# Performance work log

Hardware: AMD Instinct MI355X
Metric: run time of the kernel (lower is better)

Reference implementation:

```python
import jax, jax.numpy as jnp
import numpy as np

H = 1024       # hidden_size
R = 4          # downsacale_ratio -> bottleneck H//R = 256
DI = 2048      # mamba d_inner = expand * H
NS = 16        # d_state
KC = 4         # d_conv
DTR = 64       # dt_rank = ceil(H/16)
B, L = 4, 1024


def setup_inputs() -> dict:
    key = jax.random.key(0)
    ks = iter(jax.random.split(key, 32))
    w = lambda shape, s=0.02: jax.random.normal(next(ks), shape, jnp.float32) * s
    Hr = H // R
    inp = {
        'x': jax.random.normal(next(ks), (B, L, H), jnp.float32),
        't': jax.random.normal(next(ks), (B, H), jnp.float32),
        # adaLN modulation: SiLU -> Linear(H, 3H)
        'ada_w': w((H, 3 * H)), 'ada_b': jnp.zeros((3 * H,), jnp.float32),
        # hg_dense: Linear(H,H/R) SiLU Linear(H/R,H)
        'hgd_w1': w((H, Hr)), 'hgd_b1': jnp.zeros((Hr,), jnp.float32),
        'hgd_w2': w((Hr, H)), 'hgd_b2': jnp.zeros((H,), jnp.float32),
        # Mamba params
        'in_proj_w': w((H, 2 * DI)),
        'conv_w': w((DI, KC), 0.1), 'conv_b': jnp.zeros((DI,), jnp.float32),
        'x_proj_w': w((DI, DTR + 2 * NS)),
        'dt_proj_w': w((DTR, DI), 0.1),
        'dt_proj_b': jnp.log(jnp.expm1(jnp.full((DI,), 0.01, jnp.float32))),  # softplus^-1(0.01)
        'A_log': jnp.log(jnp.broadcast_to(jnp.arange(1, NS + 1, dtype=jnp.float32), (DI, NS))),
        'Dp': jnp.ones((DI,), jnp.float32),
        'out_proj_w': w((DI, H)),
        # hg_fuse
        'fm_w': w((H, Hr)), 'fm_b': jnp.zeros((Hr,), jnp.float32),
        'fr_w': w((H, Hr)), 'fr_b': jnp.zeros((Hr,), jnp.float32),
        'ff_w': w((Hr, H)), 'ff_b': jnp.zeros((H,), jnp.float32),
    }
    return inp


def _ln(x, eps=1e-6):
    mu = jnp.mean(x, -1, keepdims=True)
    var = jnp.mean(jnp.square(x - mu), -1, keepdims=True)
    return (x - mu) / jnp.sqrt(var + eps)


def _mamba(xd, in_proj_w, conv_w, conv_b, x_proj_w, dt_proj_w, dt_proj_b, A_log, Dp, out_proj_w):
    # xd: [B, L, H]
    xz = xd @ in_proj_w                      # [B, L, 2*DI]
    xm, z = jnp.split(xz, 2, axis=-1)
    # causal depthwise conv over time
    xc = jnp.swapaxes(xm, 1, 2)              # [B, DI, L]
    xc = jax.lax.conv_general_dilated(
        xc, conv_w[:, None, :], window_strides=(1,), padding=[(KC - 1, 0)],
        feature_group_count=DI, dimension_numbers=('NCH', 'OIH', 'NCH'))
    xc = jax.nn.silu(jnp.swapaxes(xc, 1, 2) + conv_b)   # [B, L, DI]
    dbl = xc @ x_proj_w                      # [B, L, DTR + 2*NS]
    dt = jax.nn.softplus(dbl[..., :DTR] @ dt_proj_w + dt_proj_b)   # [B, L, DI]
    Bm = dbl[..., DTR:DTR + NS]              # [B, L, NS]
    Cm = dbl[..., DTR + NS:]                 # [B, L, NS]
    A = -jnp.exp(A_log)                      # [DI, NS]

    def step(h, inp):
        dt_t, x_t, B_t, C_t = inp            # [B,DI],[B,DI],[B,NS],[B,NS]
        dA = jnp.exp(dt_t[:, :, None] * A)                       # [B, DI, NS]
        h = dA * h + (dt_t * x_t)[:, :, None] * B_t[:, None, :]
        y = jnp.einsum('bdn,bn->bd', h, C_t)
        return h, y

    h0 = jnp.zeros((xd.shape[0], DI, NS), xd.dtype)
    seq = (jnp.moveaxis(dt, 1, 0), jnp.moveaxis(xc, 1, 0),
           jnp.moveaxis(Bm, 1, 0), jnp.moveaxis(Cm, 1, 0))
    _, ys = jax.lax.scan(step, h0, seq)
    y = jnp.moveaxis(ys, 0, 1) + xc * Dp     # [B, L, DI]
    y = y * jax.nn.silu(z)
    return y @ out_proj_w                    # [B, L, H]


def reference(x, t, ada_w, ada_b, hgd_w1, hgd_b1, hgd_w2, hgd_b2,
              in_proj_w, conv_w, conv_b, x_proj_w, dt_proj_w, dt_proj_b,
              A_log, Dp, out_proj_w, fm_w, fm_b, fr_w, fr_b, ff_w, ff_b):
    ada = jax.nn.silu(t) @ ada_w + ada_b               # [B, 3H]
    shift, scale, alpha = jnp.split(ada, 3, axis=-1)
    x1 = _ln(x) * (1 + scale[:, None, :]) + shift[:, None, :]
    xd = jax.nn.silu(x1 @ hgd_w1 + hgd_b1) @ hgd_w2 + hgd_b2
    x1_2 = _mamba(xd, in_proj_w, conv_w, conv_b, x_proj_w, dt_proj_w,
                  dt_proj_b, A_log, Dp, out_proj_w)
    a = jax.nn.silu(x1_2 @ fm_w + fm_b)
    b = jax.nn.silu(x1 @ fr_w + fr_b)
    fuse = (a * b) @ ff_w + ff_b
    return x + alpha[:, None, :] * fuse
```

## Files before the change

### kernel.cpp

```cpp
#include <hip/hip_runtime.h>
#include <math.h>
#include <stdint.h>

#define H_   1024
#define HR_  256
#define DI_  2048
#define NS_  16
#define KC_  4
#define DTR_ 64
#define B_   4
#define L_   1024
#define ROWS (B_*L_)
#define H3_  3072
#define NCH_ 32
#define CL_  32
#define CLT_ 8

typedef short bf16x8 __attribute__((ext_vector_type(8)));
typedef float f32x4  __attribute__((ext_vector_type(4)));

#if __has_builtin(__builtin_amdgcn_exp2f)
#define EXP2(x) __builtin_amdgcn_exp2f(x)
#else
#define EXP2(x) __expf((x) * 0.6931471805599453f)
#endif
#define LOG2E 1.4426950408889634f

__device__ __forceinline__ float silu_f(float v) { return v / (1.f + __expf(-v)); }

__device__ __forceinline__ uint32_t pack_bf16_2(float a, float b) {
    uint32_t ua = __float_as_uint(a);
    uint32_t ub = __float_as_uint(b);
    uint32_t ra = (ua + 0x7FFFu + ((ua >> 16) & 1u)) >> 16;
    uint32_t rb = (ub + 0x7FFFu + ((ub >> 16) & 1u)) >> 16;
    return ra | (rb << 16);
}
__device__ __forceinline__ unsigned short cvt_bf16(float a) {
    uint32_t ua = __float_as_uint(a);
    return (unsigned short)((ua + 0x7FFFu + ((ua >> 16) & 1u)) >> 16);
}
__device__ __forceinline__ float bf16_to_f(unsigned short u) {
    return __uint_as_float(((uint32_t)u) << 16);
}

__device__ __forceinline__ void gload16(const short* g, short* l) {
    __builtin_amdgcn_global_load_lds(
        (const __attribute__((address_space(1))) void*)g,
        (__attribute__((address_space(3))) void*)l, 16, 0, 0);
}

#define TW_HGDFR 0ull
#define TW_HGD2  524288ull
#define TW_INPJ  786432ull
#define TW_XPJ   4980736ull
#define TW_DTPJ  5242880ull
#define TW_OPJ   5373952ull
#define TW_FM    7471104ull
#define TW_FF    7733248ull
#define TWT      7995392ull

__global__ __launch_bounds__(256) void wtrans_kernel(
    const float* __restrict__ s0, const float* __restrict__ s1,
    const float* __restrict__ s2, const float* __restrict__ s3,
    const float* __restrict__ s4, const float* __restrict__ s5,
    const float* __restrict__ s6, const float* __restrict__ s7,
    const float* __restrict__ s8, short* __restrict__ wt)
{
    int bid = blockIdx.x;
    const float* src; short* dst; int K, N, rel;
    if      (bid < 256)  { src = s0; dst = wt + TW_HGDFR;          K = 1024; N = 256;  rel = bid; }
    else if (bid < 512)  { src = s1; dst = wt + TW_HGDFR + 262144; K = 1024; N = 256;  rel = bid - 256; }
    else if (bid < 768)  { src = s2; dst = wt + TW_HGD2;           K = 256;  N = 1024; rel = bid - 512; }
    else if (bid < 4864) { src = s3; dst = wt + TW_INPJ;           K = 1024; N = 4096; rel = bid - 768; }
    else if (bid < 5120) { src = s4; dst = wt + TW_XPJ;            K = 2048; N = 96;   rel = bid - 4864; }
    else if (bid < 5248) { src = s5; dst = wt + TW_DTPJ;           K = 64;   N = 2048; rel = bid - 5120; }
    else if (bid < 7296) { src = s6; dst = wt + TW_OPJ;            K = 2048; N = 1024; rel = bid - 5248; }
    else if (bid < 7552) { src = s7; dst = wt + TW_FM;             K = 1024; N = 256;  rel = bid - 7296; }
    else                 { src = s8; dst = wt + TW_FF;             K = 256;  N = 1024; rel = bid - 7552; }
    int tkc = K >> 5;
    int tk = rel % tkc, tn = rel / tkc;

    __shared__ float ld[32][33];
    int tx = threadIdx.x & 7, ty = threadIdx.x >> 3;
    int kk = tk * 32 + ty, nn = tn * 32 + tx * 4;
    float4 v = make_float4(0.f, 0.f, 0.f, 0.f);
    if (nn < N) v = *(const float4*)&src[(size_t)kk * N + nn];
    ld[ty][tx * 4 + 0] = v.x; ld[ty][tx * 4 + 1] = v.y;
    ld[ty][tx * 4 + 2] = v.z; ld[ty][tx * 4 + 3] = v.w;
    __syncthreads();
    int nn2 = tn * 32 + ty, kk2 = tk * 32 + tx * 4;
    float a0 = ld[tx * 4 + 0][ty], a1 = ld[tx * 4 + 1][ty];
    float a2 = ld[tx * 4 + 2][ty], a3 = ld[tx * 4 + 3][ty];
    uint2 p = { pack_bf16_2(a0, a1), pack_bf16_2(a2, a3) };
    *(uint2*)&dst[(size_t)nn2 * K + kk2] = p;
}

__global__ __launch_bounds__(256) void cwt_kernel(
    const float* __restrict__ conv_w, float* __restrict__ cwt)
{
    int d = blockIdx.x * 256 + threadIdx.x;
    float4 v = *(const float4*)&conv_w[d * KC_];
    cwt[0 * DI_ + d] = v.x;
    cwt[1 * DI_ + d] = v.y;
    cwt[2 * DI_ + d] = v.z;
    cwt[3 * DI_ + d] = v.w;
}

__global__ __launch_bounds__(256) void ada_part_kernel(
    const float* __restrict__ t, const float* __restrict__ ada_w,
    float* __restrict__ part)
{
    int col = blockIdx.x * 1024 + threadIdx.x * 4;
    int b = blockIdx.y, z = blockIdx.z;
    __shared__ float st[32];
    if (threadIdx.x < 32) {
        float v = t[b * H_ + z * 32 + threadIdx.x];
        st[threadIdx.x] = silu_f(v);
    }
    __syncthreads();
    float4 acc = make_float4(0.f, 0.f, 0.f, 0.f);
    const float* w = ada_w + (size_t)(z * 32) * H3_ + col;
    #pragma unroll
    for (int k = 0; k < 32; ++k) {
        float4 wv = *(const float4*)(w + (size_t)k * H3_);
        float s = st[k];
        acc.x = fmaf(s, wv.x, acc.x);
        acc.y = fmaf(s, wv.y, acc.y);
        acc.z = fmaf(s, wv.z, acc.z);
        acc.w = fmaf(s, wv.w, acc.w);
    }
    *(float4*)&part[((size_t)z * B_ + b) * H3_ + col] = acc;
}

__global__ __launch_bounds__(256) void ada_red_kernel(
    const float* __restrict__ part, const float* __restrict__ ada_b,
    float* __restrict__ ada)
{
    int i = (blockIdx.x * 256 + threadIdx.x) * 4;
    int b = i / H3_, col = i - b * H3_;
    float4 s = make_float4(0.f, 0.f, 0.f, 0.f);
    #pragma unroll
    for (int z = 0; z < 32; ++z) {
        float4 p = *(const float4*)&part[((size_t)z * B_ + b) * H3_ + col];
        s.x += p.x; s.y += p.y; s.z += p.z; s.w += p.w;
    }
    float4 bv = *(const float4*)&ada_b[col];
    s.x += bv.x; s.y += bv.y; s.z += bv.z; s.w += bv.w;
    *(float4*)&ada[(size_t)b * H3_ + col] = s;
}

__global__ __launch_bounds__(256) void ln_mod_kernel(
    const float* __restrict__ x, const float* __restrict__ ada,
    short* __restrict__ x1b)
{
    int row = blockIdx.x;
    int b   = row >> 10;
    const float* xr = x + (size_t)row * H_;
    float4 v = ((const float4*)xr)[threadIdx.x];
    float s  = v.x + v.y + v.z + v.w;
    float s2 = v.x*v.x + v.y*v.y + v.z*v.z + v.w*v.w;

    __shared__ float red[8];
    int wave = threadIdx.x >> 6, lane = threadIdx.x & 63;
    #pragma unroll
    for (int off = 32; off; off >>= 1) {
        s  += __shfl_down(s,  off);
        s2 += __shfl_down(s2, off);
    }
    if (lane == 0) { red[wave] = s; red[4 + wave] = s2; }
    __syncthreads();
    float ts  = red[0] + red[1] + red[2] + red[3];
    float ts2 = red[4] + red[5] + red[6] + red[7];
    float mu  = ts  * (1.f / H_);
    float var = ts2 * (1.f / H_) - mu * mu;
    float inv = rsqrtf(var + 1e-6f);

    const float* sh = ada + b * H3_;
    int i = threadIdx.x * 4;
    float4 sh4 = *(const float4*)&sh[i];
    float4 sc4 = *(const float4*)&sh[H_ + i];
    float ox = (v.x - mu) * inv * (1.f + sc4.x) + sh4.x;
    float oy = (v.y - mu) * inv * (1.f + sc4.y) + sh4.y;
    float oz = (v.z - mu) * inv * (1.f + sc4.z) + sh4.z;
    float ow = (v.w - mu) * inv * (1.f + sc4.w) + sh4.w;
    uint2 p = { pack_bf16_2(ox, oy), pack_bf16_2(oz, ow) };
    *(uint2*)(x1b + (size_t)row * H_ + i) = p;
}

template<int ACT, bool SPLITK>
__global__ __launch_bounds__(256) void gemm128(
    const short* __restrict__ A, int lda,
    const short* __restrict__ Wt, int ldw,
    const float* __restrict__ bias,
    float* __restrict__ C, short* __restrict__ Cb, short* __restrict__ Cb2,
    int ldc, int M, int N, int K,
    const float* __restrict__ E0, const float* __restrict__ E1)
{
    __shared__ short As[3][4096];
    __shared__ short Bs[3][4096];
    int tid  = threadIdx.x;
    int lane = tid & 63, wv = tid >> 6, wm = wv >> 1, wn = wv & 1;
    int n0 = blockIdx.x * 128;
    int m0 = blockIdx.y * 128;

    if (SPLITK) {
        int z = blockIdx.z;
        A  += (size_t)z * K;
        Wt += (size_t)z * K;
        C  += (size_t)z * M * N;
    }

    int r = lane & 15, g = lane >> 4;
    int sA = wv * 2;
    const short* ga0 = A  + (size_t)(m0 + sA * 16 + r) * lda + g * 8;
    const short* ga1 = ga0 + (size_t)16 * lda;
    const short* gb0 = Wt + (size_t)(n0 + sA * 16 + r) * ldw + g * 8;
    const short* gb1 = gb0 + (size_t)16 * ldw;

    f32x4 acc[4][4];
    #pragma unroll
    for (int i = 0; i < 4; ++i)
        #pragma unroll
        for (int j = 0; j < 4; ++j) {
            acc[i][j][0] = 0.f; acc[i][j][1] = 0.f;
            acc[i][j][2] = 0.f; acc[i][j][3] = 0.f;
        }

    #define STAGE(buf, koff)                                    \
        do {                                                    \
            gload16(ga0 + (koff), &As[buf][sA * 512]);          \
            gload16(ga1 + (koff), &As[buf][sA * 512 + 512]);    \
            gload16(gb0 + (koff), &Bs[buf][sA * 512]);          \
            gload16(gb1 + (koff), &Bs[buf][sA * 512 + 512]);    \
        } while (0)

    #define COMPUTE(buf)                                                          \
        do {                                                                      \
            bf16x8 af[4], bfr[4];                                                 \
            _Pragma("unroll")                                                     \
            for (int i = 0; i < 4; ++i)                                           \
                af[i] = *(const bf16x8*)&As[buf][(wm * 4 + i) * 512 + lane * 8];  \
            _Pragma("unroll")                                                     \
            for (int j = 0; j < 4; ++j)                                           \
                bfr[j] = *(const bf16x8*)&Bs[buf][(wn * 4 + j) * 512 + lane * 8]; \
            _Pragma("unroll")                                                     \
            for (int i = 0; i < 4; ++i)                                           \
                _Pragma("unroll")                                                 \
                for (int j = 0; j < 4; ++j)                                       \
                    acc[i][j] = __builtin_amdgcn_mfma_f32_16x16x32_bf16(          \
                        af[i], bfr[j], acc[i][j], 0, 0, 0);                       \
        } while (0)

    int T = K >> 5;
    STAGE(0, 0);
    if (T > 1) STAGE(1, 32);
    for (int t = 0; t < T; ++t) {
        if (t + 1 < T) asm volatile("s_waitcnt vmcnt(4)" ::: "memory");
        else           asm volatile("s_waitcnt vmcnt(0)" ::: "memory");
        __builtin_amdgcn_s_barrier();
        if (t + 2 < T) STAGE((t + 2) % 3, (t + 2) * 32);
        COMPUTE(t % 3);
    }
    #undef STAGE
    #undef COMPUTE

    #pragma unroll
    for (int i = 0; i < 4; ++i) {
        int mb = m0 + wm * 64 + i * 16 + ((lane >> 4) << 2);
        #pragma unroll
        for (int j = 0; j < 4; ++j) {
            int n = n0 + wn * 64 + j * 16 + (lane & 15);
            if (n < N) {
                float bv;
                if (ACT == 6) bv = (n < 256) ? bias[n] : E0[n - 256];
                else          bv = bias ? bias[n] : 0.f;
                #pragma unroll
                for (int rr = 0; rr < 4; ++rr) {
                    int m = mb + rr;
                    float v = acc[i][j][rr] + bv;
                    size_t ci = (size_t)m * ldc + n;
                    if (ACT == 6) {
                        float sv = silu_f(v);
                        if (n < 256) Cb[(size_t)m * 256 + n]        = (short)cvt_bf16(sv);
                        else         Cb2[(size_t)m * 256 + (n-256)] = (short)cvt_bf16(sv);
                    } else {
                        if (ACT == 2) v = (v > 20.f) ? v : log1pf(__expf(v));
                        else if (ACT == 4) {
                            int bb = m >> 10;
                            v = E0[ci] + E1[bb * H3_ + 2 * H_ + n] * v;
                        }
                        if (C)  C[ci]  = v;
                        if (Cb) Cb[ci] = (short)cvt_bf16(v);
                    }
                }
            }
        }
    }
}

template<int ACT>
__global__ __launch_bounds__(512) void gemm256(
    const short* __restrict__ A, int lda,
    const short* __restrict__ Wt, int ldw,
    short* __restrict__ Cb, int M, int N, int K)
{
    extern __shared__ short lds[];
    short* Asb = lds;
    short* Bsb = lds + 24576;
    int tid  = threadIdx.x;
    int lane = tid & 63, wv = tid >> 6;
    int wm = wv >> 2, wn = wv & 3;
    int n0 = blockIdx.x * 256;
    int m0 = blockIdx.y * 256;

    int r = lane & 15, g = lane >> 4;
    int sA = wv * 2;
    const short* ga0 = A  + (size_t)(m0 + sA * 16 + r) * lda + g * 8;
    const short* ga1 = ga0 + (size_t)16 * lda;
    const short* gb0 = Wt + (size_t)(n0 + sA * 16 + r) * ldw + g * 8;
    const short* gb1 = gb0 + (size_t)16 * ldw;

    f32x4 acc[8][4];
    #pragma unroll
    for (int i = 0; i < 8; ++i)
        #pragma unroll
        for (int j = 0; j < 4; ++j) {
            acc[i][j][0] = 0.f; acc[i][j][1] = 0.f;
            acc[i][j][2] = 0.f; acc[i][j][3] = 0.f;
        }

    #define STAGE2(buf, koff)                                       \
        do {                                                        \
            gload16(ga0 + (koff), &Asb[(buf) * 8192 + sA * 512]);   \
            gload16(ga1 + (koff), &Asb[(buf) * 8192 + sA * 512 + 512]); \
            gload16(gb0 + (koff), &Bsb[(buf) * 8192 + sA * 512]);   \
            gload16(gb1 + (koff), &Bsb[(buf) * 8192 + sA * 512 + 512]); \
        } while (0)

    int T = K >> 5;
    STAGE2(0, 0);
    if (T > 1) STAGE2(1, 32);
    for (int t = 0; t < T; ++t) {
        if (t + 1 < T) asm volatile("s_waitcnt vmcnt(4)" ::: "memory");
        else           asm volatile("s_waitcnt vmcnt(0)" ::: "memory");
        __builtin_amdgcn_s_barrier();
        if (t + 2 < T) STAGE2((t + 2) % 3, (t + 2) * 32);
        {
            int buf = t % 3;
            bf16x8 af[8], bfr[4];
            #pragma unroll
            for (int i = 0; i < 8; ++i)
                af[i] = *(const bf16x8*)&Asb[buf * 8192 + (wm * 8 + i) * 512 + lane * 8];
            #pragma unroll
            for (int j = 0; j < 4; ++j)
                bfr[j] = *(const bf16x8*)&Bsb[buf * 8192 + (wn * 4 + j) * 512 + lane * 8];
            __builtin_amdgcn_s_setprio(1);
            #pragma unroll
            for (int i = 0; i < 8; ++i)
                #pragma unroll
                for (int j = 0; j < 4; ++j)
                    acc[i][j] = __builtin_amdgcn_mfma_f32_16x16x32_bf16(
                        af[i], bfr[j], acc[i][j], 0, 0, 0);
            __builtin_amdgcn_s_setprio(0);
        }
    }
    #undef STAGE2

    #pragma unroll
    for (int i = 0; i < 8; ++i) {
        int mb = m0 + wm * 128 + i * 16 + ((lane >> 4) << 2);
        #pragma unroll
        for (int j = 0; j < 4; ++j) {
            int n = n0 + wn * 64 + j * 16 + (lane & 15);
            #pragma unroll
            for (int rr = 0; rr < 4; ++rr) {
                int m = mb + rr;
                float v = acc[i][j][rr];
                if (ACT == 5) {
                    size_t idx = (n < DI_) ? ((size_t)m * DI_ + n)
                                           : ((size_t)ROWS * DI_ + (size_t)m * DI_ + (n - DI_));
                    Cb[idx] = (short)cvt_bf16(v);
                }
            }
        }
    }
}

__global__ __launch_bounds__(256) void redk_xproj(
    const float* __restrict__ part, float* __restrict__ dbl,
    short* __restrict__ dblb)
{
    size_t i = ((size_t)blockIdx.x * 256 + threadIdx.x) * 4;
    const size_t seg = (size_t)ROWS * 96;
    float4 s = *(const float4*)(part + i);
    #pragma unroll
    for (int z = 1; z < 8; ++z) {
        float4 p = *(const float4*)(part + z * seg + i);
        s.x += p.x; s.y += p.y; s.z += p.z; s.w += p.w;
    }
    *(float4*)(dbl + i) = s;
    uint2 p = { pack_bf16_2(s.x, s.y), pack_bf16_2(s.z, s.w) };
    *(uint2*)(dblb + i) = p;
}

__global__ __launch_bounds__(256) void redk_op(
    const float* __restrict__ part, short* __restrict__ x12b)
{
    size_t i = ((size_t)blockIdx.x * 256 + threadIdx.x) * 4;
    const size_t seg = (size_t)ROWS * H_;
    float4 a = *(const float4*)(part + i);
    float4 b = *(const float4*)(part + seg + i);
    uint2 p = { pack_bf16_2(a.x + b.x, a.y + b.y), pack_bf16_2(a.z + b.z, a.w + b.w) };
    *(uint2*)(x12b + i) = p;
}

__global__ __launch_bounds__(256) void redk_fm(
    const float* __restrict__ part, const float* __restrict__ fm_b,
    const short* __restrict__ frlin, short* __restrict__ abb)
{
    size_t i = ((size_t)blockIdx.x * 256 + threadIdx.x) * 4;
    const size_t seg = (size_t)ROWS * HR_;
    float4 s = *(const float4*)(part + i);
    #pragma unroll
    for (int z = 1; z < 4; ++z) {
        float4 p = *(const float4*)(part + z * seg + i);
        s.x += p.x; s.y += p.y; s.z += p.z; s.w += p.w;
    }
    int col = (int)(i & (HR_ - 1));
    float4 b = *(const float4*)(fm_b + col);
    const short* fr = frlin + i;
    float o0 = silu_f(s.x + b.x) * bf16_to_f((unsigned short)fr[0]);
    float o1 = silu_f(s.y + b.y) * bf16_to_f((unsigned short)fr[1]);
    float o2 = silu_f(s.z + b.z) * bf16_to_f((unsigned short)fr[2]);
    float o3 = silu_f(s.w + b.w) * bf16_to_f((unsigned short)fr[3]);
    uint2 p = { pack_bf16_2(o0, o1), pack_bf16_2(o2, o3) };
    *(uint2*)(abb + i) = p;
}

__global__ __launch_bounds__(256) void conv_kernel(
    const short* __restrict__ xmb, const float* __restrict__ cwt,
    const float* __restrict__ conv_b, short* __restrict__ xcb)
{
    int d0 = threadIdx.x * 8;
    int b  = blockIdx.y;
    int l0 = blockIdx.x * CLT_;

    float w[KC_][8];
    #pragma unroll
    for (int j = 0; j < KC_; ++j) {
        float4 a = *(const float4*)&cwt[j * DI_ + d0];
        float4 c = *(const float4*)&cwt[j * DI_ + d0 + 4];
        w[j][0] = a.x; w[j][1] = a.y; w[j][2] = a.z; w[j][3] = a.w;
        w[j][4] = c.x; w[j][5] = c.y; w[j][6] = c.z; w[j][7] = c.w;
    }
    float bia[8];
    {
        float4 b0 = *(const float4*)&conv_b[d0];
        float4 b1 = *(const float4*)&conv_b[d0 + 4];
        bia[0] = b0.x; bia[1] = b0.y; bia[2] = b0.z; bia[3] = b0.w;
        bia[4] = b1.x; bia[5] = b1.y; bia[6] = b1.z; bia[7] = b1.w;
    }

    const short* base = xmb + (size_t)b * L_ * DI_ + d0;
    short*       outb = xcb + (size_t)b * L_ * DI_ + d0;

    bf16x8 win[KC_];
    #pragma unroll
    for (int j = 0; j < KC_ - 1; ++j) {
        int ll = l0 - (KC_ - 1) + j;
        if (ll >= 0) win[j] = *(const bf16x8*)(base + (size_t)ll * DI_);
        else         win[j] = (bf16x8)0;
    }
    for (int l = l0; l < l0 + CLT_; ++l) {
        win[KC_ - 1] = *(const bf16x8*)(base + (size_t)l * DI_);
        bf16x8 o;
        #pragma unroll
        for (int e = 0; e < 8; ++e) {
            float acc = bia[e];
            #pragma unroll
            for (int j = 0; j < KC_; ++j)
                acc = fmaf(bf16_to_f((unsigned short)win[j][e]), w[j][e], acc);
            o[e] = (short)cvt_bf16(silu_f(acc));
        }
        *(bf16x8*)(outb + (size_t)l * DI_) = o;
        win[0] = win[1]; win[1] = win[2]; win[2] = win[3];
    }
}

__global__ __launch_bounds__(256) void scan_part1(
    const short* __restrict__ dtb, const short* __restrict__ xcb,
    const float* __restrict__ dbl, const float* __restrict__ A_log,
    float* __restrict__ hend, float* __restrict__ dtsum)
{
    int bx = blockIdx.x;
    int dg = bx & 15;
    int bc = bx >> 4;
    int c  = bc & (NCH_ - 1);
    int b  = bc >> 5;
    int tid  = threadIdx.x;
    int lane = tid & 63, wv = tid >> 6;
    int dl   = tid >> 1;
    int d    = dg * 128 + dl;
    int half = tid & 1;
    int n0   = half * 8;

    __shared__ float sB[CL_][NS_];
    __shared__ short dtS[2][16][128];
    __shared__ short xcS[2][16][128];

    size_t srcoff = (size_t)(b * L_ + c * CL_ + wv * 4 + (lane >> 4)) * DI_
                    + dg * 128 + (lane & 15) * 8;
    const short* gdt = dtb + srcoff;
    const short* gxc = xcb + srcoff;

    #define SSTG1(buf, q)                                             \
        do {                                                          \
            gload16(gdt + (size_t)(q) * 16 * DI_, &dtS[buf][wv*4][0]); \
            gload16(gxc + (size_t)(q) * 16 * DI_, &xcS[buf][wv*4][0]); \
        } while (0)

    SSTG1(0, 0);
    for (int idx = tid; idx < CL_ * NS_; idx += 256) {
        int l = idx >> 4, n = idx & 15;
        sB[l][n] = dbl[(size_t)(b * L_ + c * CL_ + l) * 96 + DTR_ + n];
    }
    float Aa2[8];
    #pragma unroll
    for (int n = 0; n < 8; ++n)
        Aa2[n] = -__expf(A_log[d * NS_ + n0 + n]) * LOG2E;

    float h[8];
    #pragma unroll
    for (int n = 0; n < 8; ++n) h[n] = 0.f;
    float sdt = 0.f;

    __syncthreads();
    int buf = 0;
    for (int q = 0; q < 2; ++q) {
        if (q < 1) SSTG1(buf ^ 1, q + 1);
        #pragma unroll
        for (int li = 0; li < 16; ++li) {
            int l = q * 16 + li;
            float dtv = bf16_to_f((unsigned short)dtS[buf][li][dl]);
            float xv  = bf16_to_f((unsigned short)xcS[buf][li][dl]);
            float du  = dtv * xv;
            sdt += dtv;
            #pragma unroll
            for (int n = 0; n < 8; ++n)
                h[n] = fmaf(EXP2(dtv * Aa2[n]), h[n], du * sB[l][n0 + n]);
        }
        __syncthreads();
        buf ^= 1;
    }
    #undef SSTG1

    #pragma unroll
    for (int n = 0; n < 8; ++n)
        hend[((size_t)((b * NCH_ + c) * NS_ + n0 + n)) * DI_ + d] = h[n];
    if (half == 0)
        dtsum[(size_t)(b * NCH_ + c) * DI_ + d] = sdt;
}

__global__ __launch_bounds__(256) void scan_mid(
    const float* __restrict__ hend, const float* __restrict__ dtsum,
    const float* __restrict__ A_log, float* __restrict__ hin)
{
    int idx = blockIdx.x * 256 + threadIdx.x;
    int d  = idx & (DI_ - 1);
    int bn = idx >> 11;
    int n  = bn & (NS_ - 1);
    int b  = bn >> 4;
    float Aa2 = -__expf(A_log[d * NS_ + n]) * LOG2E;
    float h = 0.f;
    #pragma unroll
    for (int c = 0; c < NCH_; ++c) {
        size_t o = ((size_t)((b * NCH_ + c) * NS_ + n)) * DI_ + d;
        hin[o] = h;
        float s = dtsum[(size_t)(b * NCH_ + c) * DI_ + d];
        h = fmaf(EXP2(Aa2 * s), h, hend[o]);
    }
}

__global__ __launch_bounds__(256) void scan_part2(
    const short* __restrict__ dtb, const short* __restrict__ xcb,
    const short* __restrict__ zb, const float* __restrict__ dbl,
    const float* __restrict__ A_log, const float* __restrict__ Dp,
    const float* __restrict__ hin, short* __restrict__ y2b)
{
    int bx = blockIdx.x;
    int dg = bx & 15;
    int bc = bx >> 4;
    int c  = bc & (NCH_ - 1);
    int b  = bc >> 5;
    int tid  = threadIdx.x;
    int lane = tid & 63, wv = tid >> 6;
    int dl   = tid >> 1;
    int d    = dg * 128 + dl;
    int half = tid & 1;
    int n0   = half * 8;

    __shared__ float sBC[CL_][2 * NS_];
    __shared__ short dtS[2][16][128];
    __shared__ short xcS[2][16][128];
    __shared__ short zS[2][16][128];

    size_t srcoff = (size_t)(b * L_ + c * CL_ + wv * 4 + (lane >> 4)) * DI_
                    + dg * 128 + (lane & 15) * 8;
    const short* gdt = dtb + srcoff;
    const short* gxc = xcb + srcoff;
    const short* gz  = zb  + srcoff;

    #define SSTG2(buf, q)                                             \
        do {                                                          \
            gload16(gdt + (size_t)(q) * 16 * DI_, &dtS[buf][wv*4][0]); \
            gload16(gxc + (size_t)(q) * 16 * DI_, &xcS[buf][wv*4][0]); \
            gload16(gz  + (size_t)(q) * 16 * DI_, &zS[buf][wv*4][0]);  \
        } while (0)

    SSTG2(0, 0);
    for (int idx = tid; idx < CL_ * 2 * NS_; idx += 256) {
        int l = idx >> 5, n = idx & 31;
        sBC[l][n] = dbl[(size_t)(b * L_ + c * CL_ + l) * 96 + DTR_ + n];
    }
    float Aa2[8];
    #pragma unroll
    for (int n = 0; n < 8; ++n)
        Aa2[n] = -__expf(A_log[d * NS_ + n0 + n]) * LOG2E;

    float h[8];
    #pragma unroll
    for (int n = 0; n < 8; ++n)
        h[n] = hin[((size_t)((b * NCH_ + c) * NS_ + n0 + n)) * DI_ + d];
    float Dpv = Dp[d];
    size_t obase = (size_t)(b * L_ + c * CL_) * DI_ + d;

    __syncthreads();
    int buf = 0;
    for (int q = 0; q < 2; ++q) {
        if (q < 1) SSTG2(buf ^ 1, q + 1);
        #pragma unroll
        for (int li = 0; li < 16; ++li) {
            int l = q * 16 + li;
            float dtv = bf16_to_f((unsigned short)dtS[buf][li][dl]);
            float xv  = bf16_to_f((unsigned short)xcS[buf][li][dl]);
            float zv  = bf16_to_f((unsigned short)zS[buf][li][dl]);
            float du  = dtv * xv;
            float y = 0.f;
            #pragma unroll
            for (int n = 0; n < 8; ++n) {
                float dA = EXP2(dtv * Aa2[n]);
                h[n] = fmaf(dA, h[n], du * sBC[l][n0 + n]);
                y = fmaf(h[n], sBC[l][NS_ + n0 + n], y);
            }
            y += __shfl_xor(y, 1);
            if (half == 0) {
                y = fmaf(xv, Dpv, y);
                y2b[obase + (size_t)l * DI_] = (short)cvt_bf16(y * silu_f(zv));
            }
        }
        __syncthreads();
        buf ^= 1;
    }
    #undef SSTG2
}

extern "C" void kernel_launch(void* const* d_in, const int* in_sizes, int n_in,
                              void* d_out, int out_size, void* d_ws, size_t ws_size,
                              hipStream_t stream)
{
    const float* x         = (const float*)d_in[0];
    const float* t         = (const float*)d_in[1];
    const float* ada_w     = (const float*)d_in[2];
    const float* ada_b     = (const float*)d_in[3];
    const float* hgd_w1    = (const float*)d_in[4];
    const float* hgd_b1    = (const float*)d_in[5];
    const float* hgd_w2    = (const float*)d_in[6];
    const float* hgd_b2    = (const float*)d_in[7];
    const float* in_proj_w = (const float*)d_in[8];
    const float* conv_w    = (const float*)d_in[9];
    const float* conv_b    = (const float*)d_in[10];
    const float* x_proj_w  = (const float*)d_in[11];
    const float* dt_proj_w = (const float*)d_in[12];
    const float* dt_proj_b = (const float*)d_in[13];
    const float* A_log     = (const float*)d_in[14];
    const float* Dp        = (const float*)d_in[15];
    const float* out_proj_w= (const float*)d_in[16];
    const float* fm_w      = (const float*)d_in[17];
    const float* fm_b      = (const float*)d_in[18];
    const float* fr_w      = (const float*)d_in[19];
    const float* fr_b      = (const float*)d_in[20];
    const float* ff_w      = (const float*)d_in[21];
    const float* ff_b      = (const float*)d_in[22];
    float* out = (float*)d_out;

    char* p = (char*)d_ws;
    auto alloc = [&](size_t bytes) { char* r = p; p += (bytes + 255) & ~255ull; return r; };

    short* wt      = (short*)alloc(TWT * 2);
    float* cwt     = (float*)alloc((size_t)KC_ * DI_ * 4);
    short* x1b     = (short*)alloc((size_t)ROWS * H_ * 2);
    short* h1b     = (short*)alloc((size_t)ROWS * HR_ * 2);
    short* frlin   = (short*)alloc((size_t)ROWS * HR_ * 2);
    short* xdb     = (short*)alloc((size_t)ROWS * H_ * 2);
    short* xmzb    = (short*)alloc((size_t)ROWS * DI_ * 4);
    short* xcb     = (short*)alloc((size_t)ROWS * DI_ * 2);
    short* y2b     = (short*)alloc((size_t)ROWS * DI_ * 2);
    short* dtb     = (short*)alloc((size_t)ROWS * DI_ * 2);
    float* bigpart = (float*)alloc((size_t)2 * ROWS * H_ * 4);
    float* hend    = (float*)alloc((size_t)B_ * NCH_ * NS_ * DI_ * 4);
    float* dbl     = (float*)alloc((size_t)ROWS * 96 * 4);
    short* dblb    = (short*)alloc((size_t)ROWS * 96 * 2);
    short* x12b    = (short*)alloc((size_t)ROWS * H_ * 2);
    short* abb     = (short*)alloc((size_t)ROWS * HR_ * 2);
    float* ada     = (float*)alloc((size_t)B_ * H3_ * 4);

    short* xmb   = xmzb;
    short* zb    = xmzb + (size_t)ROWS * DI_;
    float* dtsum = (float*)abb;
    float* hin   = bigpart;
    float* adapart = bigpart;

    dim3 blk(256), b512(512);

    wtrans_kernel<<<dim3(7808), blk, 0, stream>>>(
        hgd_w1, fr_w, hgd_w2, in_proj_w, x_proj_w, dt_proj_w, out_proj_w,
        fm_w, ff_w, wt);
    cwt_kernel<<<dim3(DI_ / 256), blk, 0, stream>>>(conv_w, cwt);
    ada_part_kernel<<<dim3(3, B_, 32), blk, 0, stream>>>(t, ada_w, adapart);
    ada_red_kernel<<<dim3(B_ * H3_ / 4 / 256), blk, 0, stream>>>(adapart, ada_b, ada);
    ln_mod_kernel<<<dim3(ROWS), blk, 0, stream>>>(x, ada, x1b);
    gemm128<6, false><<<dim3(4, 32), blk, 0, stream>>>(
        x1b, H_, wt + TW_HGDFR, H_, hgd_b1, nullptr, h1b, frlin,
        512, ROWS, 512, H_, fr_b, nullptr);
    gemm128<0, false><<<dim3(8, 32), blk, 0, stream>>>(
        h1b, HR_, wt + TW_HGD2, HR_, hgd_b2, nullptr, xdb, nullptr,
        H_, ROWS, H_, HR_, nullptr, nullptr);
    gemm256<5><<<dim3(16, 16), b512, 98304, stream>>>(
        xdb, H_, wt + TW_INPJ, H_, xmb, ROWS, 2 * DI_, H_);
    conv_kernel<<<dim3(L_ / CLT_, B_), blk, 0, stream>>>(xmb, cwt, conv_b, xcb);
    gemm128<0, true><<<dim3(1, 32, 8), blk, 0, stream>>>(
        xcb, DI_, wt + TW_XPJ, DI_, nullptr, bigpart, nullptr, nullptr,
        96, ROWS, 96, 256, nullptr, nullptr);
    redk_xproj<<<dim3(ROWS * 96 / 4 / 256), blk, 0, stream>>>(bigpart, dbl, dblb);
    gemm128<2, false><<<dim3(16, 32), blk, 0, stream>>>(
        dblb, 96, wt + TW_DTPJ, DTR_, dt_proj_b, nullptr, dtb, nullptr,
        DI_, ROWS, DI_, DTR_, nullptr, nullptr);
    scan_part1<<<dim3(B_ * NCH_ * 16), blk, 0, stream>>>(
        dtb, xcb, dbl, A_log, hend, dtsum);
    scan_mid<<<dim3(B_ * DI_ * NS_ / 256), blk, 0, stream>>>(
        hend, dtsum, A_log, hin);
    scan_part2<<<dim3(B_ * NCH_ * 16), blk, 0, stream>>>(
        dtb, xcb, zb, dbl, A_log, Dp, hin, y2b);
    gemm128<0, true><<<dim3(8, 32, 2), blk, 0, stream>>>(
        y2b, DI_, wt + TW_OPJ, DI_, nullptr, bigpart, nullptr, nullptr,
        H_, ROWS, H_, 1024, nullptr, nullptr);
    redk_op<<<dim3(ROWS * H_ / 4 / 256), blk, 0, stream>>>(bigpart, x12b);
    gemm128<0, true><<<dim3(2, 32, 4), blk, 0, stream>>>(
        x12b, H_, wt + TW_FM, H_, nullptr, bigpart, nullptr, nullptr,
        HR_, ROWS, HR_, 256, nullptr, nullptr);
    redk_fm<<<dim3(ROWS * HR_ / 4 / 256), blk, 0, stream>>>(bigpart, fm_b, frlin, abb);
    gemm128<4, false><<<dim3(8, 32), blk, 0, stream>>>(
        abb, HR_, wt + TW_FF, HR_, ff_b, out, nullptr, nullptr,
        H_, ROWS, H_, HR_, x, ada);
}
```

Baseline: 361.2 us.

## Use K=64 staged 256-tile GEMM for in_proj and split-K 256-tile out_proj

Adds a gemm256k64 variant that stages 64-wide K slices into double-buffered LDS (128 KB) for the in_proj GEMM, halving the number of barrier/stage iterations. The out_proj GEMM switches from a 128-tile split-K=2 kernel to the 256-tile kernel with split-K=4 and fp32 partial outputs, followed by a 4-way reduction kernel. Workspace is consolidated into one scratch buffer sized for four partial outputs. The larger LDS footprint limits occupancy, and the extra split-K partials add memory traffic for the reduction.

```diff
diff --git a/kernel.cpp b/kernel.cpp
--- a/kernel.cpp
+++ b/kernel.cpp
@@ -298,11 +298,12 @@
     }
 }
 
-template<int ACT>
+template<int ACT, bool SPLITK>
 __global__ __launch_bounds__(512) void gemm256(
     const short* __restrict__ A, int lda,
     const short* __restrict__ Wt, int ldw,
-    short* __restrict__ Cb, int M, int N, int K)
+    short* __restrict__ Cb, float* __restrict__ C, int ldc,
+    int M, int N, int K)
 {
     extern __shared__ short lds[];
     short* Asb = lds;
@@ -312,6 +313,13 @@
     int wm = wv >> 2, wn = wv & 3;
     int n0 = blockIdx.x * 256;
     int m0 = blockIdx.y * 256;
+
+    if (SPLITK) {
+        int z = blockIdx.z;
+        A  += (size_t)z * K;
+        Wt += (size_t)z * K;
+        C  += (size_t)z * M * N;
+    }
 
     int r = lane & 15, g = lane >> 4;
     int sA = wv * 2;
@@ -380,6 +388,117 @@
                     size_t idx = (n < DI_) ? ((size_t)m * DI_ + n)
                                            : ((size_t)ROWS * DI_ + (size_t)m * DI_ + (n - DI_));
                     Cb[idx] = (short)cvt_bf16(v);
+                } else if (ACT == 7) {
+                    C[(size_t)m * ldc + n] = v;
+                }
+            }
+        }
+    }
+}
+
+template<int ACT>
+__global__ __launch_bounds__(512) void gemm256k64(
+    const short* __restrict__ A, int lda,
+    const short* __restrict__ Wt, int ldw,
+    short* __restrict__ Cb, int M, int N, int K)
+{
+    extern __shared__ short lds[];
+    short* Asb = lds;
+    short* Bsb = lds + 32768;
+    int tid  = threadIdx.x;
+    int lane = tid & 63, wv = tid >> 6;
+    int wm = wv >> 2, wn = wv & 3;
+    int n0 = blockIdx.x * 256;
+    int m0 = blockIdx.y * 256;
+
+    const short* gaP0; const short* gaP1; const short* gaP2; const short* gaP3;
+    const short* gbP0; const short* gbP1; const short* gbP2; const short* gbP3;
+    int lo0, lo1, lo2, lo3;
+    {
+        int f0 = wv, f1 = 8 + wv, f2 = 16 + wv, f3 = 24 + wv;
+        #define SRC(fi, P, base, ld)                                              \
+            P = base + (size_t)((fi >> 1) * 16 + (lane & 15)) * ld                \
+                     + (fi & 1) * 32 + (lane >> 4) * 8;
+        SRC(f0, gaP0, (A + (size_t)m0 * lda), lda)  lo0 = f0 * 512;
+        SRC(f1, gaP1, (A + (size_t)m0 * lda), lda)  lo1 = f1 * 512;
+        SRC(f2, gaP2, (A + (size_t)m0 * lda), lda)  lo2 = f2 * 512;
+        SRC(f3, gaP3, (A + (size_t)m0 * lda), lda)  lo3 = f3 * 512;
+        SRC(f0, gbP0, (Wt + (size_t)n0 * ldw), ldw)
+        SRC(f1, gbP1, (Wt + (size_t)n0 * ldw), ldw)
+        SRC(f2, gbP2, (Wt + (size_t)n0 * ldw), ldw)
+        SRC(f3, gbP3, (Wt + (size_t)n0 * ldw), ldw)
+        #undef SRC
+    }
+
+    f32x4 acc[8][4];
+    #pragma unroll
+    for (int i = 0; i < 8; ++i)
+        #pragma unroll
+        for (int j = 0; j < 4; ++j) {
+            acc[i][j][0] = 0.f; acc[i][j][1] = 0.f;
+            acc[i][j][2] = 0.f; acc[i][j][3] = 0.f;
+        }
+
+    #define STAGE64(buf, koff)                                  \
+        do {                                                    \
+            gload16(gaP0 + (koff), &Asb[(buf) * 16384 + lo0]);  \
+            gload16(gaP1 + (koff), &Asb[(buf) * 16384 + lo1]);  \
+            gload16(gaP2 + (koff), &Asb[(buf) * 16384 + lo2]);  \
+            gload16(gaP3 + (koff), &Asb[(buf) * 16384 + lo3]);  \
+            gload16(gbP0 + (koff), &Bsb[(buf) * 16384 + lo0]);  \
+            gload16(gbP1 + (koff), &Bsb[(buf) * 16384 + lo1]);  \
+            gload16(gbP2 + (koff), &Bsb[(buf) * 16384 + lo2]);  \
+            gload16(gbP3 + (koff), &Bsb[(buf) * 16384 + lo3]);  \
+        } while (0)
+
+    int T = K >> 6;
+    STAGE64(0, 0);
+    int cur = 0;
+    for (int t = 0; t < T; ++t) {
+        if (t + 1 < T) {
+            STAGE64(cur ^ 1, (t + 1) * 64);
+            asm volatile("s_waitcnt vmcnt(8)" ::: "memory");
+        } else {
+            asm volatile("s_waitcnt vmcnt(0)" ::: "memory");
+        }
+        __builtin_amdgcn_s_barrier();
+        #pragma unroll
+        for (int kh = 0; kh < 2; ++kh) {
+            bf16x8 af[8], bfr[4];
+            #pragma unroll
+            for (int i = 0; i < 8; ++i)
+                af[i] = *(const bf16x8*)&Asb[cur * 16384 + (((wm * 8 + i) << 1) + kh) * 512 + lane * 8];
+            #pragma unroll
+            for (int j = 0; j < 4; ++j)
+                bfr[j] = *(const bf16x8*)&Bsb[cur * 16384 + (((wn * 4 + j) << 1) + kh) * 512 + lane * 8];
+            __builtin_amdgcn_s_setprio(1);
+            #pragma unroll
+            for (int i = 0; i < 8; ++i)
+                #pragma unroll
+                for (int j = 0; j < 4; ++j)
+                    acc[i][j] = __builtin_amdgcn_mfma_f32_16x16x32_bf16(
+                        af[i], bfr[j], acc[i][j], 0, 0, 0);
+            __builtin_amdgcn_s_setprio(0);
+        }
+        __builtin_amdgcn_s_barrier();
+        cur ^= 1;
+    }
+    #undef STAGE64
+
+    #pragma unroll
+    for (int i = 0; i < 8; ++i) {
+        int mb = m0 + wm * 128 + i * 16 + ((lane >> 4) << 2);
+        #pragma unroll
+        for (int j = 0; j < 4; ++j) {
+            int n = n0 + wn * 64 + j * 16 + (lane & 15);
+            #pragma unroll
+            for (int rr = 0; rr < 4; ++rr) {
+                int m = mb + rr;
+                float v = acc[i][j][rr];
+                if (ACT == 5) {
+                    size_t idx = (n < DI_) ? ((size_t)m * DI_ + n)
+                                           : ((size_t)ROWS * DI_ + (size_t)m * DI_ + (n - DI_));
+                    Cb[idx] = (short)cvt_bf16(v);
                 }
             }
         }
@@ -403,14 +522,18 @@
     *(uint2*)(dblb + i) = p;
 }
 
-__global__ __launch_bounds__(256) void redk_op(
+__global__ __launch_bounds__(256) void redk_op4(
     const float* __restrict__ part, short* __restrict__ x12b)
 {
     size_t i = ((size_t)blockIdx.x * 256 + threadIdx.x) * 4;
     const size_t seg = (size_t)ROWS * H_;
-    float4 a = *(const float4*)(part + i);
-    float4 b = *(const float4*)(part + seg + i);
-    uint2 p = { pack_bf16_2(a.x + b.x, a.y + b.y), pack_bf16_2(a.z + b.z, a.w + b.w) };
+    float4 s = *(const float4*)(part + i);
+    #pragma unroll
+    for (int z = 1; z < 4; ++z) {
+        float4 p = *(const float4*)(part + z * seg + i);
+        s.x += p.x; s.y += p.y; s.z += p.z; s.w += p.w;
+    }
+    uint2 p = { pack_bf16_2(s.x, s.y), pack_bf16_2(s.z, s.w) };
     *(uint2*)(x12b + i) = p;
 }
 
@@ -706,8 +829,7 @@
     short* xcb     = (short*)alloc((size_t)ROWS * DI_ * 2);
     short* y2b     = (short*)alloc((size_t)ROWS * DI_ * 2);
     short* dtb     = (short*)alloc((size_t)ROWS * DI_ * 2);
-    float* bigpart = (float*)alloc((size_t)2 * ROWS * H_ * 4);
-    float* hend    = (float*)alloc((size_t)B_ * NCH_ * NS_ * DI_ * 4);
+    float* scratch = (float*)alloc((size_t)4 * ROWS * H_ * 4);
     float* dbl     = (float*)alloc((size_t)ROWS * 96 * 4);
     short* dblb    = (short*)alloc((size_t)ROWS * 96 * 2);
     short* x12b    = (short*)alloc((size_t)ROWS * H_ * 2);
@@ -717,8 +839,12 @@
     short* xmb   = xmzb;
     short* zb    = xmzb + (size_t)ROWS * DI_;
     float* dtsum = (float*)abb;
-    float* hin   = bigpart;
-    float* adapart = bigpart;
+    float* adapart = scratch;
+    float* xppart  = scratch;
+    float* hend    = scratch;
+    float* hin     = scratch + (size_t)B_ * NCH_ * NS_ * DI_;
+    float* oppart  = scratch;
+    float* fmpart  = scratch;
 
     dim3 blk(256), b512(512);
 
@@ -735,13 +861,13 @@
     gemm128<0, false><<<dim3(8, 32), blk, 0, stream>>>(
         h1b, HR_, wt + TW_HGD2, HR_, hgd_b2, nullptr, xdb, nullptr,
         H_, ROWS, H_, HR_, nullptr, nullptr);
-    gemm256<5><<<dim3(16, 16), b512, 98304, stream>>>(
+    gemm256k64<5><<<dim3(16, 16), b512, 131072, stream>>>(
         xdb, H_, wt + TW_INPJ, H_, xmb, ROWS, 2 * DI_, H_);
     conv_kernel<<<dim3(L_ / CLT_, B_), blk, 0, stream>>>(xmb, cwt, conv_b, xcb);
     gemm128<0, true><<<dim3(1, 32, 8), blk, 0, stream>>>(
-        xcb, DI_, wt + TW_XPJ, DI_, nullptr, bigpart, nullptr, nullptr,
+        xcb, DI_, wt + TW_XPJ, DI_, nullptr, xppart, nullptr, nullptr,
         96, ROWS, 96, 256, nullptr, nullptr);
-    redk_xproj<<<dim3(ROWS * 96 / 4 / 256), blk, 0, stream>>>(bigpart, dbl, dblb);
+    redk_xproj<<<dim3(ROWS * 96 / 4 / 256), blk, 0, stream>>>(xppart, dbl, dblb);
     gemm128<2, false><<<dim3(16, 32), blk, 0, stream>>>(
         dblb, 96, wt + TW_DTPJ, DTR_, dt_proj_b, nullptr, dtb, nullptr,
         DI_, ROWS, DI_, DTR_, nullptr, nullptr);
@@ -751,14 +877,13 @@
         hend, dtsum, A_log, hin);
     scan_part2<<<dim3(B_ * NCH_ * 16), blk, 0, stream>>>(
         dtb, xcb, zb, dbl, A_log, Dp, hin, y2b);
-    gemm128<0, true><<<dim3(8, 32, 2), blk, 0, stream>>>(
-        y2b, DI_, wt + TW_OPJ, DI_, nullptr, bigpart, nullptr, nullptr,
-        H_, ROWS, H_, 1024, nullptr, nullptr);
-    redk_op<<<dim3(ROWS * H_ / 4 / 256), blk, 0, stream>>>(bigpart, x12b);
+    gemm256<7, true><<<dim3(4, 16, 4), b512, 98304, stream>>>(
+        y2b, DI_, wt + TW_OPJ, DI_, nullptr, oppart, H_, ROWS, H_, 512);
+    redk_op4<<<dim3(ROWS * H_ / 4 / 256), blk, 0, stream>>>(oppart, x12b);
     gemm128<0, true><<<dim3(2, 32, 4), blk, 0, stream>>>(
-        x12b, H_, wt + TW_FM, H_, nullptr, bigpart, nullptr, nullptr,
+        x12b, H_, wt + TW_FM, H_, nullptr, fmpart, nullptr, nullptr,
         HR_, ROWS, HR_, 256, nullptr, nullptr);
-    redk_fm<<<dim3(ROWS * HR_ / 4 / 256), blk, 0, stream>>>(bigpart, fm_b, frlin, abb);
+    redk_fm<<<dim3(ROWS * HR_ / 4 / 256), blk, 0, stream>>>(fmpart, fm_b, frlin, abb);
     gemm128<4, false><<<dim3(8, 32), blk, 0, stream>>>(
         abb, HR_, wt + TW_FF, HR_, ff_b, out, nullptr, nullptr,
         H_, ROWS, H_, HR_, x, ada);
```

Result: no change. 359.9 us (-0.4%).

## Use 256-tile double-buffered GEMM with 4-way split-K bf16 partials for out_proj

Applied to the files above, without the earlier changes.

The 256x256 GEMM now uses two LDS buffers with __syncthreads instead of a three-stage vmcnt-gated pipeline, cutting LDS from 96KB to 64KB. The same kernel gains a split-K mode that runs out_proj as 4 K-slices of 512, writing bf16 partial sums. A new reducer sums the four bf16 partials into x12b, replacing the fp32 two-way split-K reducer. Workspace buffers are merged into one scratch region. The aim is larger tiles and less reduction traffic for out_proj, at the cost of extra bf16 rounding in the partials and a shallower in_proj pipeline.

```diff
diff --git a/kernel.cpp b/kernel.cpp
--- a/kernel.cpp
+++ b/kernel.cpp
@@ -298,20 +298,28 @@
     }
 }
 
-template<int ACT>
-__global__ __launch_bounds__(512) void gemm256(
+template<int ACT, bool SPLITK>
+__global__ __launch_bounds__(512) void gemm256d(
     const short* __restrict__ A, int lda,
     const short* __restrict__ Wt, int ldw,
-    short* __restrict__ Cb, int M, int N, int K)
+    short* __restrict__ Cb, int ldc,
+    int M, int N, int K)
 {
     extern __shared__ short lds[];
     short* Asb = lds;
-    short* Bsb = lds + 24576;
+    short* Bsb = lds + 16384;
     int tid  = threadIdx.x;
     int lane = tid & 63, wv = tid >> 6;
     int wm = wv >> 2, wn = wv & 3;
     int n0 = blockIdx.x * 256;
     int m0 = blockIdx.y * 256;
+
+    if (SPLITK) {
+        int z = blockIdx.z;
+        A  += (size_t)z * K;
+        Wt += (size_t)z * K;
+        Cb += (size_t)z * M * N;
+    }
 
     int r = lane & 15, g = lane >> 4;
     int sA = wv * 2;
@@ -339,21 +347,18 @@
 
     int T = K >> 5;
     STAGE2(0, 0);
-    if (T > 1) STAGE2(1, 32);
+    __syncthreads();
+    int cur = 0;
     for (int t = 0; t < T; ++t) {
-        if (t + 1 < T) asm volatile("s_waitcnt vmcnt(4)" ::: "memory");
-        else           asm volatile("s_waitcnt vmcnt(0)" ::: "memory");
-        __builtin_amdgcn_s_barrier();
-        if (t + 2 < T) STAGE2((t + 2) % 3, (t + 2) * 32);
+        if (t + 1 < T) STAGE2(cur ^ 1, (t + 1) * 32);
         {
-            int buf = t % 3;
             bf16x8 af[8], bfr[4];
             #pragma unroll
             for (int i = 0; i < 8; ++i)
-                af[i] = *(const bf16x8*)&Asb[buf * 8192 + (wm * 8 + i) * 512 + lane * 8];
+                af[i] = *(const bf16x8*)&Asb[cur * 8192 + (wm * 8 + i) * 512 + lane * 8];
             #pragma unroll
             for (int j = 0; j < 4; ++j)
-                bfr[j] = *(const bf16x8*)&Bsb[buf * 8192 + (wn * 4 + j) * 512 + lane * 8];
+                bfr[j] = *(const bf16x8*)&Bsb[cur * 8192 + (wn * 4 + j) * 512 + lane * 8];
             __builtin_amdgcn_s_setprio(1);
             #pragma unroll
             for (int i = 0; i < 8; ++i)
@@ -363,6 +368,8 @@
                         af[i], bfr[j], acc[i][j], 0, 0, 0);
             __builtin_amdgcn_s_setprio(0);
         }
+        __syncthreads();
+        cur ^= 1;
     }
     #undef STAGE2
 
@@ -380,6 +387,8 @@
                     size_t idx = (n < DI_) ? ((size_t)m * DI_ + n)
                                            : ((size_t)ROWS * DI_ + (size_t)m * DI_ + (n - DI_));
                     Cb[idx] = (short)cvt_bf16(v);
+                } else if (ACT == 8) {
+                    Cb[(size_t)m * ldc + n] = (short)cvt_bf16(v);
                 }
             }
         }
@@ -403,15 +412,25 @@
     *(uint2*)(dblb + i) = p;
 }
 
-__global__ __launch_bounds__(256) void redk_op(
-    const float* __restrict__ part, short* __restrict__ x12b)
-{
-    size_t i = ((size_t)blockIdx.x * 256 + threadIdx.x) * 4;
+__global__ __launch_bounds__(256) void redk_op4(
+    const short* __restrict__ part, short* __restrict__ x12b)
+{
+    size_t i = ((size_t)blockIdx.x * 256 + threadIdx.x) * 8;
     const size_t seg = (size_t)ROWS * H_;
-    float4 a = *(const float4*)(part + i);
-    float4 b = *(const float4*)(part + seg + i);
-    uint2 p = { pack_bf16_2(a.x + b.x, a.y + b.y), pack_bf16_2(a.z + b.z, a.w + b.w) };
-    *(uint2*)(x12b + i) = p;
+    float s[8];
+    bf16x8 p0 = *(const bf16x8*)(part + i);
+    #pragma unroll
+    for (int e = 0; e < 8; ++e) s[e] = bf16_to_f((unsigned short)p0[e]);
+    #pragma unroll
+    for (int z = 1; z < 4; ++z) {
+        bf16x8 pz = *(const bf16x8*)(part + z * seg + i);
+        #pragma unroll
+        for (int e = 0; e < 8; ++e) s[e] += bf16_to_f((unsigned short)pz[e]);
+    }
+    bf16x8 o;
+    #pragma unroll
+    for (int e = 0; e < 8; ++e) o[e] = (short)cvt_bf16(s[e]);
+    *(bf16x8*)(x12b + i) = o;
 }
 
 __global__ __launch_bounds__(256) void redk_fm(
@@ -706,8 +725,7 @@
     short* xcb     = (short*)alloc((size_t)ROWS * DI_ * 2);
     short* y2b     = (short*)alloc((size_t)ROWS * DI_ * 2);
     short* dtb     = (short*)alloc((size_t)ROWS * DI_ * 2);
-    float* bigpart = (float*)alloc((size_t)2 * ROWS * H_ * 4);
-    float* hend    = (float*)alloc((size_t)B_ * NCH_ * NS_ * DI_ * 4);
+    float* scratch = (float*)alloc((size_t)4 * ROWS * H_ * 4);
     float* dbl     = (float*)alloc((size_t)ROWS * 96 * 4);
     short* dblb    = (short*)alloc((size_t)ROWS * 96 * 2);
     short* x12b    = (short*)alloc((size_t)ROWS * H_ * 2);
@@ -717,8 +735,12 @@
     short* xmb   = xmzb;
     short* zb    = xmzb + (size_t)ROWS * DI_;
     float* dtsum = (float*)abb;
-    float* hin   = bigpart;
-    float* adapart = bigpart;
+    float* adapart = scratch;
+    float* xppart  = scratch;
+    float* hend    = scratch;
+    float* hin     = scratch + (size_t)B_ * NCH_ * NS_ * DI_;
+    short* oppart  = (short*)scratch;
+    float* fmpart  = scratch;
 
     dim3 blk(256), b512(512);
 
@@ -735,13 +757,13 @@
     gemm128<0, false><<<dim3(8, 32), blk, 0, stream>>>(
         h1b, HR_, wt + TW_HGD2, HR_, hgd_b2, nullptr, xdb, nullptr,
         H_, ROWS, H_, HR_, nullptr, nullptr);
-    gemm256<5><<<dim3(16, 16), b512, 98304, stream>>>(
-        xdb, H_, wt + TW_INPJ, H_, xmb, ROWS, 2 * DI_, H_);
+    gemm256d<5, false><<<dim3(16, 16), b512, 65536, stream>>>(
+        xdb, H_, wt + TW_INPJ, H_, xmb, 2 * DI_, ROWS, 2 * DI_, H_);
     conv_kernel<<<dim3(L_ / CLT_, B_), blk, 0, stream>>>(xmb, cwt, conv_b, xcb);
     gemm128<0, true><<<dim3(1, 32, 8), blk, 0, stream>>>(
-        xcb, DI_, wt + TW_XPJ, DI_, nullptr, bigpart, nullptr, nullptr,
+        xcb, DI_, wt + TW_XPJ, DI_, nullptr, xppart, nullptr, nullptr,
         96, ROWS, 96, 256, nullptr, nullptr);
-    redk_xproj<<<dim3(ROWS * 96 / 4 / 256), blk, 0, stream>>>(bigpart, dbl, dblb);
+    redk_xproj<<<dim3(ROWS * 96 / 4 / 256), blk, 0, stream>>>(xppart, dbl, dblb);
     gemm128<2, false><<<dim3(16, 32), blk, 0, stream>>>(
         dblb, 96, wt + TW_DTPJ, DTR_, dt_proj_b, nullptr, dtb, nullptr,
         DI_, ROWS, DI_, DTR_, nullptr, nullptr);
@@ -751,14 +773,13 @@
         hend, dtsum, A_log, hin);
     scan_part2<<<dim3(B_ * NCH_ * 16), blk, 0, stream>>>(
         dtb, xcb, zb, dbl, A_log, Dp, hin, y2b);
-    gemm128<0, true><<<dim3(8, 32, 2), blk, 0, stream>>>(
-        y2b, DI_, wt + TW_OPJ, DI_, nullptr, bigpart, nullptr, nullptr,
-        H_, ROWS, H_, 1024, nullptr, nullptr);
-    redk_op<<<dim3(ROWS * H_ / 4 / 256), blk, 0, stream>>>(bigpart, x12b);
+    gemm256d<8, true><<<dim3(4, 16, 4), b512, 65536, stream>>>(
+        y2b, DI_, wt + TW_OPJ, DI_, oppart, H_, ROWS, H_, 512);
+    redk_op4<<<dim3(ROWS * H_ / 8 / 256), blk, 0, stream>>>(oppart, x12b);
     gemm128<0, true><<<dim3(2, 32, 4), blk, 0, stream>>>(
-        x12b, H_, wt + TW_FM, H_, nullptr, bigpart, nullptr, nullptr,
+        x12b, H_, wt + TW_FM, H_, nullptr, fmpart, nullptr, nullptr,
         HR_, ROWS, HR_, 256, nullptr, nullptr);
-    redk_fm<<<dim3(ROWS * HR_ / 4 / 256), blk, 0, stream>>>(bigpart, fm_b, frlin, abb);
+    redk_fm<<<dim3(ROWS * HR_ / 4 / 256), blk, 0, stream>>>(fmpart, fm_b, frlin, abb);
     gemm128<4, false><<<dim3(8, 32), blk, 0, stream>>>(
         abb, HR_, wt + TW_FF, HR_, ff_b, out, nullptr, nullptr,
         H_, ROWS, H_, HR_, x, ada);
```

Result: faster. 352.1 us (-2.5%).
